# Optimization experiments

Hardware: AMD Instinct MI355X
Metric: run time of the kernel (lower is better)

The kernel has to match this reference:

```python
import jax, jax.numpy as jnp
import numpy as np

NEG_INF = -1e30
EPS = 1e-6


def _apply_rope_interleaved(x, cos, sin):
    # x: (..., rope_dim); cos/sin broadcastable to (..., rope_dim//2)
    x1 = x[..., 0::2]
    x2 = x[..., 1::2]
    o1 = x1 * cos - x2 * sin
    o2 = x1 * sin + x2 * cos
    return jnp.stack([o1, o2], axis=-1).reshape(x.shape)


def setup_inputs() -> dict:
    key = jax.random.key(0)
    ks = jax.random.split(key, 6)
    B, S, D = 1, 2048, 7168
    H, HD, ROPE, QLR = 64, 128, 64, 1536
    x = jax.random.normal(ks[0], (B, S, D), dtype=jnp.float32)
    q_lora = jax.random.normal(ks[1], (B, S, QLR), dtype=jnp.float32)
    wq_b = jax.random.normal(ks[2], (QLR, H * HD), dtype=jnp.float32) * 0.02
    wk = jax.random.normal(ks[3], (D, HD), dtype=jnp.float32) * 0.02
    weights_proj = jax.random.normal(ks[4], (D, H), dtype=jnp.float32) * 0.02
    k_norm_w = jnp.ones((HD,), dtype=jnp.float32)
    k_norm_b = jnp.zeros((HD,), dtype=jnp.float32)
    # standard RoPE tables for the first ROPE dims
    half = ROPE // 2
    inv_freq = 1.0 / (10000.0 ** (np.arange(half, dtype=np.float64) / half))
    ang = np.arange(S, dtype=np.float64)[:, None] * inv_freq[None, :]
    cos = jnp.asarray(np.cos(ang), dtype=jnp.float32)
    sin = jnp.asarray(np.sin(ang), dtype=jnp.float32)
    return {"x": x, "q_lora": q_lora, "wq_b": wq_b, "wk": wk,
            "weights_proj": weights_proj, "k_norm_w": k_norm_w,
            "k_norm_b": k_norm_b, "cos": cos, "sin": sin, "topk": 512}


def reference(x, q_lora, wq_b, wk, weights_proj, k_norm_w, k_norm_b, cos, sin, topk):
    B, S, D = x.shape
    HD = wk.shape[1]
    H = weights_proj.shape[1]
    ROPE = cos.shape[1] * 2
    # queries: low-rank up-projection -> per-head, RoPE on first ROPE dims
    q = (q_lora @ wq_b).reshape(B, S, H, HD)
    q_pe = _apply_rope_interleaved(q[..., :ROPE], cos[None, :, None, :], sin[None, :, None, :])
    q = jnp.concatenate([q_pe, q[..., ROPE:]], axis=-1)
    # keys: single head, LayerNorm then RoPE on first ROPE dims
    k = x @ wk  # [B,S,HD]
    mu = k.mean(-1, keepdims=True)
    var = ((k - mu) ** 2).mean(-1, keepdims=True)
    k = (k - mu) * jax.lax.rsqrt(var + EPS) * k_norm_w + k_norm_b
    k_pe = _apply_rope_interleaved(k[..., :ROPE], cos[None], sin[None])
    k = jnp.concatenate([k_pe, k[..., ROPE:]], axis=-1)
    # per-token head gates, scaled by n_heads^-0.5 and softmax scale HD^-0.5
    w = (x @ weights_proj) * (H ** -0.5) * (HD ** -0.5)  # [B,S,H]
    # lightning index score: I[t,s] = sum_h w[t,h] * relu(q[t,h] . k[s])
    scores = jax.nn.relu(jnp.einsum('bshd,btd->bsht', q, k))  # [B,S,H,S]
    index_score = jnp.einsum('bsht,bsh->bst', scores, w)      # [B,S,S]
    # causal mask then top-k token selection
    causal = jnp.arange(S)[None, :] <= jnp.arange(S)[:, None]
    index_score = jnp.where(causal[None], index_score, NEG_INF)
    vals, idx = jax.lax.top_k(index_score, topk)
    return vals, idx
```

## Files before the change

### kernel.cpp

```cpp
#include <hip/hip_runtime.h>
#include <stdint.h>

#define S_LEN 2048
#define D_DIM 7168
#define H_NUM 64
#define HD_DIM 128
#define QLR_DIM 1536
#define NQ_DIM 8192
#define ROPE_DIM 64
#define HALF_DIM 32
#define TOPK_N 512
#define NEG_INF_F (-1e30f)
#define LN_EPS 1e-6f
#define W_SCALE 0.011048543456039806f

#define KCHUNKS 7
#define KCHUNK_SZ 1024

#define QF_HSTRIDE (128 * 4 * 64 * 8)

#define QBF_OFF 0
#define ALORA_OFF (QBF_OFF + S_LEN * NQ_DIM / 2)
#define WT_OFF   (ALORA_OFF + S_LEN * QLR_DIM / 2)
#define XBF_OFF  (WT_OFF + NQ_DIM * QLR_DIM / 2)
#define WT2_OFF  (XBF_OFF + S_LEN * D_DIM / 2)
#define KF_OFF   (WT2_OFF + 192 * D_DIM / 2)
#define KBF_OFF  (KF_OFF + S_LEN * HD_DIM)
#define WF_OFF   (KBF_OFF + S_LEN * HD_DIM / 2)
#define SC_OFF   (WF_OFF + S_LEN * H_NUM)

typedef __attribute__((ext_vector_type(8))) short short8;
typedef __attribute__((ext_vector_type(4))) float floatx4;

__device__ __forceinline__ ushort f2bf(float f) {
    unsigned int u = __float_as_uint(f);
    u += 0x7FFFu + ((u >> 16) & 1u);
    return (ushort)(u >> 16);
}
__device__ __forceinline__ unsigned int pack2bf(float lo, float hi) {
    return (unsigned int)f2bf(lo) | ((unsigned int)f2bf(hi) << 16);
}

__device__ __forceinline__ void gld_lds16(const ushort* g, ushort* l) {
    __builtin_amdgcn_global_load_lds(
        (const __attribute__((address_space(1))) unsigned int*)g,
        (__attribute__((address_space(3))) unsigned int*)l, 16, 0, 0);
}

__global__ __launch_bounds__(256) void cast_bf16_kernel(
    const float* __restrict__ in, ushort* __restrict__ out)
{
    int g = (blockIdx.x * 256 + threadIdx.x) * 8;
    float4 a = *(const float4*)&in[g];
    float4 b = *(const float4*)&in[g + 4];
    uint4 v;
    v.x = pack2bf(a.x, a.y); v.y = pack2bf(a.z, a.w);
    v.z = pack2bf(b.x, b.y); v.w = pack2bf(b.z, b.w);
    *(uint4*)&out[g] = v;
}

__global__ __launch_bounds__(256) void transpose_wqb_kernel(
    const float* __restrict__ W, ushort* __restrict__ WT)
{
    __shared__ ushort tl[64][72];
    const int n0 = blockIdx.x * 64, k0 = blockIdx.y * 64;
    const int t = threadIdx.x;
    const int r = t >> 4, c4 = (t & 15) * 4;
#pragma unroll
    for (int u = 0; u < 4; u++) {
        int kk = r + u * 16;
        float4 v = *(const float4*)&W[(size_t)(k0 + kk) * NQ_DIM + n0 + c4];
        tl[c4 + 0][kk] = f2bf(v.x);
        tl[c4 + 1][kk] = f2bf(v.y);
        tl[c4 + 2][kk] = f2bf(v.z);
        tl[c4 + 3][kk] = f2bf(v.w);
    }
    __syncthreads();
#pragma unroll
    for (int u = 0; u < 2; u++) {
        int i = t + u * 256;
        int nr = i >> 3, c8 = (i & 7) * 8;
        uint4 v = *(const uint4*)&tl[nr][c8];
        *(uint4*)&WT[(size_t)(n0 + nr) * QLR_DIM + k0 + c8] = v;
    }
}

__global__ __launch_bounds__(256) void transpose_wkp_kernel(
    const float* __restrict__ WK, const float* __restrict__ WP,
    ushort* __restrict__ WT2)
{
    __shared__ ushort tl[64][72];
    const int ntile = blockIdx.x;
    const int k0 = blockIdx.y * 64;
    const float* src; int ld, cbase;
    if (ntile < 2) { src = WK; ld = HD_DIM; cbase = ntile * 64; }
    else           { src = WP; ld = H_NUM; cbase = 0; }
    const int t = threadIdx.x;
    const int r = t >> 4, c4 = (t & 15) * 4;
#pragma unroll
    for (int u = 0; u < 4; u++) {
        int kk = r + u * 16;
        float4 v = *(const float4*)&src[(size_t)(k0 + kk) * ld + cbase + c4];
        tl[c4 + 0][kk] = f2bf(v.x);
        tl[c4 + 1][kk] = f2bf(v.y);
        tl[c4 + 2][kk] = f2bf(v.z);
        tl[c4 + 3][kk] = f2bf(v.w);
    }
    __syncthreads();
#pragma unroll
    for (int u = 0; u < 2; u++) {
        int i = t + u * 256;
        int nr = i >> 3, c8 = (i & 7) * 8;
        uint4 v = *(const uint4*)&tl[nr][c8];
        *(uint4*)&WT2[(size_t)(ntile * 64 + nr) * D_DIM + k0 + c8] = v;
    }
}

__global__ __launch_bounds__(256) void qgemm_mfma_kernel(
    const ushort* __restrict__ Abf,
    const ushort* __restrict__ WT,
    const float* __restrict__ cosp, const float* __restrict__ sinp,
    ushort* __restrict__ Qo)
{
    __shared__ ushort lds[128 * 136];
    ushort* As = lds;
    ushort* Bs = lds + 4096;

    const int tid = threadIdx.x;
    const int lane = tid & 63;
    const int wave = tid >> 6;
    const int m = lane & 15;
    const int q = lane >> 4;
    const int wm = wave & 1, wn = wave >> 1;
    const int m0 = blockIdx.y * 128;
    const int n0 = blockIdx.x * 128;
    const int h = blockIdx.x;

    floatx4 acc[4][4];
#pragma unroll
    for (int i = 0; i < 4; i++)
#pragma unroll
        for (int j = 0; j < 4; j++) acc[i][j] = (floatx4){0.f, 0.f, 0.f, 0.f};

    const ushort* agp[2];
    const ushort* bgp[2];
    unsigned int sbase[2];
#pragma unroll
    for (int u = 0; u < 2; u++) {
        int s = (u * 4 + wave) * 64 + lane;
        agp[u] = Abf + (size_t)(m0 + (s >> 2)) * QLR_DIM + (s & 3) * 8;
        bgp[u] = WT + (size_t)(n0 + (s >> 2)) * QLR_DIM + (s & 3) * 8;
        sbase[u] = (unsigned int)((u * 4 + wave) * 64 * 8);
    }

    for (int kt = 0; kt < QLR_DIM; kt += 32) {
        __syncthreads();
#pragma unroll
        for (int u = 0; u < 2; u++) gld_lds16(agp[u] + kt, &As[sbase[u]]);
#pragma unroll
        for (int u = 0; u < 2; u++) gld_lds16(bgp[u] + kt, &Bs[sbase[u]]);
        __syncthreads();

        short8 af[4], bf[4];
#pragma unroll
        for (int mt = 0; mt < 4; mt++)
            af[mt] = *(const short8*)&As[(wm * 64 + mt * 16 + m) * 32 + q * 8];
#pragma unroll
        for (int nt = 0; nt < 4; nt++)
            bf[nt] = *(const short8*)&Bs[(wn * 64 + nt * 16 + m) * 32 + q * 8];
#pragma unroll
        for (int mt = 0; mt < 4; mt++)
#pragma unroll
            for (int nt = 0; nt < 4; nt++)
                acc[mt][nt] = __builtin_amdgcn_mfma_f32_16x16x32_bf16(
                    af[mt], bf[nt], acc[mt][nt], 0, 0, 0);
    }

    __syncthreads();
    ushort* ep = lds;

#pragma unroll
    for (int mt = 0; mt < 4; mt++) {
        const int srow_base = m0 + wm * 64 + mt * 16 + q * 4;
#pragma unroll
        for (int nt = 0; nt < 4; nt++) {
            const int d = wn * 64 + nt * 16 + m;
            float o[4];
            if (wn == 0) {
                const int jj = d >> 1;
#pragma unroll
                for (int r = 0; r < 4; r++) {
                    float x = acc[mt][nt][r];
                    float p = __shfl_xor(x, 1, 64);
                    float c = cosp[(srow_base + r) * HALF_DIM + jj];
                    float sn = sinp[(srow_base + r) * HALF_DIM + jj];
                    o[r] = (d & 1) ? (p * sn + x * c) : (x * c - p * sn);
                }
            } else {
#pragma unroll
                for (int r = 0; r < 4; r++) o[r] = acc[mt][nt][r];
            }
#pragma unroll
            for (int r = 0; r < 4; r++)
                ep[(wm * 64 + mt * 16 + q * 4 + r) * 136 + d] = f2bf(o[r]);
        }
    }
    __syncthreads();

    const int sgrp0 = m0 >> 4;
#pragma unroll
    for (int u = 0; u < 8; u++) {
        int i = u * 256 + tid;
        int sgl = i >> 8, c = i & 255;
        int ks = c >> 6, ln = c & 63;
        int srow = sgl * 16 + (ln & 15);
        int d0 = (ks << 5) + ((ln >> 4) << 3);
        uint4 v = *(const uint4*)&ep[srow * 136 + d0];
        size_t dst = (size_t)h * QF_HSTRIDE +
                     ((((size_t)(sgrp0 + sgl) * 4 + ks) * 64 + ln) * 8);
        *(uint4*)&Qo[dst] = v;
    }
}

__global__ __launch_bounds__(256) void kw_mfma_kernel(
    const ushort* __restrict__ Xbf,
    const ushort* __restrict__ WT2,
    float* __restrict__ partial)
{
    __shared__ ushort As[128 * 64];
    __shared__ ushort Bs[64 * 64];

    const int tid = threadIdx.x;
    const int lane = tid & 63;
    const int wave = tid >> 6;
    const int m = lane & 15;
    const int q = lane >> 4;
    const int wm = wave & 1, wn = wave >> 1;
    const int m0 = blockIdx.x * 128;
    const int n0 = blockIdx.y * 64;
    const int kc = blockIdx.z;
    const size_t kbase = (size_t)kc * KCHUNK_SZ;

    const ushort* agp[4];
    unsigned int abase[4];
#pragma unroll
    for (int u = 0; u < 4; u++) {
        int s = (u * 4 + wave) * 64 + lane;
        int row = s >> 3, c = s & 7;
        int kg = c ^ (row & 7);
        agp[u] = Xbf + (size_t)(m0 + row) * D_DIM + kbase + kg * 8;
        abase[u] = (unsigned int)((u * 4 + wave) * 64 * 8);
    }
    const ushort* bgp[2];
    unsigned int bbase[2];
#pragma unroll
    for (int u = 0; u < 2; u++) {
        int s = (u * 4 + wave) * 64 + lane;
        int row = s >> 3, c = s & 7;
        int kg = c ^ (row & 7);
        bgp[u] = WT2 + (size_t)(n0 + row) * D_DIM + kbase + kg * 8;
        bbase[u] = (unsigned int)((u * 4 + wave) * 64 * 8);
    }

    floatx4 acc[4][2];
#pragma unroll
    for (int i = 0; i < 4; i++)
#pragma unroll
        for (int j = 0; j < 2; j++) acc[i][j] = (floatx4){0.f, 0.f, 0.f, 0.f};

    for (int kt = 0; kt < KCHUNK_SZ; kt += 64) {
        __syncthreads();
#pragma unroll
        for (int u = 0; u < 4; u++) gld_lds16(agp[u] + kt, &As[abase[u]]);
#pragma unroll
        for (int u = 0; u < 2; u++) gld_lds16(bgp[u] + kt, &Bs[bbase[u]]);
        __syncthreads();

        short8 af[4][2], bfr[2][2];
#pragma unroll
        for (int mt = 0; mt < 4; mt++) {
            int row = wm * 64 + mt * 16 + m;
#pragma unroll
            for (int ks = 0; ks < 2; ks++)
                af[mt][ks] = *(const short8*)
                    &As[row * 64 + ((((ks << 2) + q) ^ (m & 7)) * 8)];
        }
#pragma unroll
        for (int nt = 0; nt < 2; nt++) {
            int row = wn * 32 + nt * 16 + m;
#pragma unroll
            for (int ks = 0; ks < 2; ks++)
                bfr[nt][ks] = *(const short8*)
                    &Bs[row * 64 + ((((ks << 2) + q) ^ (m & 7)) * 8)];
        }
#pragma unroll
        for (int mt = 0; mt < 4; mt++)
#pragma unroll
            for (int nt = 0; nt < 2; nt++)
#pragma unroll
                for (int ks = 0; ks < 2; ks++)
                    acc[mt][nt] = __builtin_amdgcn_mfma_f32_16x16x32_bf16(
                        af[mt][ks], bfr[nt][ks], acc[mt][nt], 0, 0, 0);
    }

#pragma unroll
    for (int mt = 0; mt < 4; mt++) {
        int grow = m0 + wm * 64 + mt * 16 + q * 4;
#pragma unroll
        for (int nt = 0; nt < 2; nt++) {
            int gn = n0 + wn * 32 + nt * 16 + m;
#pragma unroll
            for (int r = 0; r < 4; r++)
                partial[((size_t)kc * S_LEN + grow + r) * 192 + gn] = acc[mt][nt][r];
        }
    }
}

__global__ __launch_bounds__(256) void kw_reduce_kernel(
    const float* __restrict__ partial, float* __restrict__ Ko, float* __restrict__ Wo)
{
    int g = blockIdx.x * 256 + threadIdx.x;
    int m = g / 192, n = g % 192;
    float s = 0.f;
#pragma unroll
    for (int c = 0; c < KCHUNKS; c++)
        s += partial[((size_t)c * S_LEN + m) * 192 + n];
    if (n < HD_DIM) Ko[(size_t)m * HD_DIM + n] = s;
    else            Wo[(size_t)m * H_NUM + (n - HD_DIM)] = s * W_SCALE;
}

__global__ __launch_bounds__(128) void knorm_rope_kernel(
    const float* __restrict__ Kf, const float* __restrict__ gw, const float* __restrict__ gb,
    const float* __restrict__ cosp, const float* __restrict__ sinp,
    ushort* __restrict__ Kbf)
{
    __shared__ float red[128];
    __shared__ float sh[128];
    const int m = blockIdx.x, t = threadIdx.x;
    float v = Kf[(size_t)m * HD_DIM + t];
    red[t] = v; __syncthreads();
    for (int off = 64; off > 0; off >>= 1) {
        if (t < off) red[t] += red[t + off];
        __syncthreads();
    }
    float mu = red[0] * (1.f / HD_DIM);
    __syncthreads();
    float dv = v - mu;
    red[t] = dv * dv; __syncthreads();
    for (int off = 64; off > 0; off >>= 1) {
        if (t < off) red[t] += red[t + off];
        __syncthreads();
    }
    float var = red[0] * (1.f / HD_DIM);
    float rs = rsqrtf(var + LN_EPS);
    float kn = dv * rs * gw[t] + gb[t];
    sh[t] = kn; __syncthreads();
    float out;
    if (t < ROPE_DIM) {
        int jj = t >> 1;
        float c = cosp[m * HALF_DIM + jj], sn = sinp[m * HALF_DIM + jj];
        out = ((t & 1) == 0) ? (sh[t] * c - sh[t + 1] * sn)
                             : (sh[t - 1] * sn + sh[t] * c);
    } else {
        out = kn;
    }
    Kbf[(size_t)m * HD_DIM + t] = f2bf(out);
}

__global__ __launch_bounds__(256, 2) void attn_mfma_kernel(
    const ushort* __restrict__ Qb,
    const ushort* __restrict__ Kb,
    const float* __restrict__ Wf,
    float* __restrict__ SC)
{
    __shared__ float Wsm[64 * 68];

    const int bidx = blockIdx.x;
    const int x = bidx & 7, j = bidx >> 3;
    const int g1 = x + 1, g2 = 32 - x, g3 = x + 9;
    int ts, tt;
    if (j < g1)                { ts = x;      tt = j; }
    else if (j < g1 + g2)      { ts = 31 - x; tt = j - g1; }
    else if (j < g1 + g2 + g3) { ts = x + 8;  tt = j - g1 - g2; }
    else                       { ts = 23 - x; tt = j - g1 - g2 - g3; }
    const int s0 = ts * 64, t0 = tt * 64;

    const int tid = threadIdx.x;
    const int lane = tid & 63;
    const int m = lane & 15;
    const int q = lane >> 4;
    const int strip = (tid >> 6) * 16;

    {
        const float4* gw = (const float4*)(Wf + (size_t)s0 * H_NUM);
#pragma unroll
        for (int u = 0; u < 4; u++) {
            int ch = tid + u * 256;
            float4 v = gw[ch];
            *(float4*)&Wsm[(ch >> 4) * 68 + (ch & 15) * 4] = v;
        }
    }

    short8 bf[4][4];
#pragma unroll
    for (int tile = 0; tile < 4; tile++)
#pragma unroll
        for (int ks = 0; ks < 4; ks++)
            bf[tile][ks] = *(const short8*)
                &Kb[(size_t)(t0 + tile * 16 + m) * HD_DIM + ks * 32 + q * 8];

    __syncthreads();

    float acc[4][4];
#pragma unroll
    for (int tile = 0; tile < 4; tile++)
#pragma unroll
        for (int r = 0; r < 4; r++) acc[tile][r] = 0.f;

    const int sgrp = ts * 4 + (strip >> 4);
    const ushort* qfb = Qb + ((size_t)sgrp * 4 * 64 + lane) * 8;
    const float* wrow = &Wsm[(strip + q * 4) * 68];

    auto loadQ = [&](short8* dst, int h) {
        const ushort* p = qfb + (size_t)h * QF_HSTRIDE;
#pragma unroll
        for (int ks = 0; ks < 4; ks++) dst[ks] = *(const short8*)&p[ks * 512];
    };
    auto computeH = [&](const short8* af, int h) {
        float wv[4];
#pragma unroll
        for (int r = 0; r < 4; r++) wv[r] = wrow[r * 68 + h];
#pragma unroll
        for (int tile = 0; tile < 4; tile++) {
            floatx4 p = {0.f, 0.f, 0.f, 0.f};
#pragma unroll
            for (int ks = 0; ks < 4; ks++)
                p = __builtin_amdgcn_mfma_f32_16x16x32_bf16(af[ks], bf[tile][ks], p, 0, 0, 0);
#pragma unroll
            for (int r = 0; r < 4; r++)
                acc[tile][r] += fmaxf(p[r], 0.f) * wv[r];
        }
    };

    short8 afA[4], afB[4];
    loadQ(afA, 0);
    for (int h = 0; h < H_NUM; h += 2) {
        loadQ(afB, h + 1);
        computeH(afA, h);
        if (h + 2 < H_NUM) loadQ(afA, h + 2);
        computeH(afB, h + 1);
    }

#pragma unroll
    for (int tile = 0; tile < 4; tile++)
#pragma unroll
        for (int r = 0; r < 4; r++)
            SC[(size_t)(s0 + strip + q * 4 + r) * S_LEN + t0 + tile * 16 + m] =
                acc[tile][r];
}

__device__ __forceinline__ unsigned int fkey(float f) {
    unsigned int u = __float_as_uint(f);
    return (u & 0x80000000u) ? ~u : (u | 0x80000000u);
}
__device__ __forceinline__ float fdec(unsigned int k) {
    unsigned int u = (k & 0x80000000u) ? (k & 0x7FFFFFFFu) : ~k;
    return __uint_as_float(u);
}

__global__ __launch_bounds__(256) void topk_kernel(
    const float* __restrict__ SC, float* __restrict__ outv, float* __restrict__ outi)
{
    __shared__ unsigned long long key[S_LEN];
    const int s = blockIdx.x, tid = threadIdx.x;
    for (int t = tid; t < S_LEN; t += 256) {
        float v = (t <= s) ? SC[(size_t)s * S_LEN + t] : NEG_INF_F;
        key[t] = ((unsigned long long)fkey(v) << 32) |
                 (unsigned long long)(unsigned int)(S_LEN - 1 - t);
    }
    __syncthreads();
    for (int k2 = 2; k2 <= S_LEN; k2 <<= 1) {
        for (int j = k2 >> 1; j > 0; j >>= 1) {
            for (int p = tid; p < S_LEN / 2; p += 256) {
                int i = 2 * p - (p & (j - 1));
                int ix = i + j;
                unsigned long long a = key[i], b = key[ix];
                bool up = ((i & k2) == 0);
                bool sw = up ? (a < b) : (a > b);
                if (sw) { key[i] = b; key[ix] = a; }
            }
            __syncthreads();
        }
    }
    for (int i2 = tid; i2 < TOPK_N; i2 += 256) {
        unsigned long long kv = key[i2];
        outv[(size_t)s * TOPK_N + i2] = fdec((unsigned int)(kv >> 32));
        outi[(size_t)s * TOPK_N + i2] =
            (float)(S_LEN - 1 - (int)(kv & 0xFFFFFFFFu));
    }
}

extern "C" void kernel_launch(void* const* d_in, const int* in_sizes, int n_in,
                              void* d_out, int out_size, void* d_ws, size_t ws_size,
                              hipStream_t stream)
{
    (void)in_sizes; (void)n_in; (void)out_size; (void)ws_size;
    const float* x      = (const float*)d_in[0];
    const float* q_lora = (const float*)d_in[1];
    const float* wq_b   = (const float*)d_in[2];
    const float* wk     = (const float*)d_in[3];
    const float* wproj  = (const float*)d_in[4];
    const float* knw    = (const float*)d_in[5];
    const float* knb    = (const float*)d_in[6];
    const float* cosp   = (const float*)d_in[7];
    const float* sinp   = (const float*)d_in[8];

    float* ws = (float*)d_ws;
    ushort* Qbf  = (ushort*)(ws + QBF_OFF);
    ushort* Albf = (ushort*)(ws + ALORA_OFF);
    ushort* WTbf = (ushort*)(ws + WT_OFF);
    ushort* Xbf  = (ushort*)(ws + XBF_OFF);
    ushort* WT2  = (ushort*)(ws + WT2_OFF);
    float*  Kf   = ws + KF_OFF;
    ushort* Kbf  = (ushort*)(ws + KBF_OFF);
    float*  Wf   = ws + WF_OFF;
    float*  SCb  = ws + SC_OFF;
    float*  partial = ws + SC_OFF;

    float* outv = (float*)d_out;
    float* outi = outv + (size_t)S_LEN * TOPK_N;

    cast_bf16_kernel<<<(S_LEN * QLR_DIM) / (256 * 8), 256, 0, stream>>>(q_lora, Albf);
    cast_bf16_kernel<<<(S_LEN * D_DIM) / (256 * 8), 256, 0, stream>>>(x, Xbf);
    transpose_wqb_kernel<<<dim3(NQ_DIM / 64, QLR_DIM / 64), 256, 0, stream>>>(wq_b, WTbf);
    transpose_wkp_kernel<<<dim3(3, D_DIM / 64), 256, 0, stream>>>(wk, wproj, WT2);
    kw_mfma_kernel<<<dim3(S_LEN / 128, 3, KCHUNKS), 256, 0, stream>>>(Xbf, WT2, partial);
    kw_reduce_kernel<<<(S_LEN * 192) / 256, 256, 0, stream>>>(partial, Kf, Wf);
    knorm_rope_kernel<<<S_LEN, 128, 0, stream>>>(Kf, knw, knb, cosp, sinp, Kbf);
    qgemm_mfma_kernel<<<dim3(NQ_DIM / 128, S_LEN / 128), 256, 0, stream>>>(
        Albf, WTbf, cosp, sinp, Qbf);
    attn_mfma_kernel<<<528, 256, 0, stream>>>(Qbf, Kbf, Wf, SCb);
    topk_kernel<<<S_LEN, 256, 0, stream>>>(SCb, outv, outi);
}
```

Measured before the change: 401.8 us.

## Replace full bitonic sort with chunked 512-sort and merge using 32-bit packed keys

The top-k kernel now sorts only the causally active prefix of each row, split into 512-element chunks. Each chunk is bitonic-sorted, then chunks are merged pairwise keeping the top 512. Keys shrink from 64-bit to 32-bit by packing a truncated float key with an 11-bit index, and output values are read back from a saved value array. This cuts shared-memory traffic and sort stages, especially for early rows. In exchange, ordering can deviate when scores differ only in the truncated low mantissa bits.

Result: faster. 361.1 us (-10.1%).

```diff
diff --git a/kernel.cpp b/kernel.cpp
--- a/kernel.cpp
+++ b/kernel.cpp
@@ -463,40 +463,57 @@
     unsigned int u = __float_as_uint(f);
     return (u & 0x80000000u) ? ~u : (u | 0x80000000u);
 }
-__device__ __forceinline__ float fdec(unsigned int k) {
-    unsigned int u = (k & 0x80000000u) ? (k & 0x7FFFFFFFu) : ~k;
-    return __uint_as_float(u);
-}
 
 __global__ __launch_bounds__(256) void topk_kernel(
     const float* __restrict__ SC, float* __restrict__ outv, float* __restrict__ outi)
 {
-    __shared__ unsigned long long key[S_LEN];
+    __shared__ unsigned int key[S_LEN];
+    __shared__ float val[S_LEN];
     const int s = blockIdx.x, tid = threadIdx.x;
-    for (int t = tid; t < S_LEN; t += 256) {
+    const int nchunks = (s >> 9) + 1;
+    const int nact = nchunks << 9;
+
+    for (int t = tid; t < nact; t += 256) {
         float v = (t <= s) ? SC[(size_t)s * S_LEN + t] : NEG_INF_F;
-        key[t] = ((unsigned long long)fkey(v) << 32) |
-                 (unsigned long long)(unsigned int)(S_LEN - 1 - t);
-    }
-    __syncthreads();
-    for (int k2 = 2; k2 <= S_LEN; k2 <<= 1) {
+        val[t] = v;
+        key[t] = (fkey(v) & 0xFFFFF800u) | (unsigned int)(S_LEN - 1 - t);
+    }
+    __syncthreads();
+
+    for (int k2 = 2; k2 <= 512; k2 <<= 1) {
         for (int j = k2 >> 1; j > 0; j >>= 1) {
-            for (int p = tid; p < S_LEN / 2; p += 256) {
+            for (int p = tid; p < (nact >> 1); p += 256) {
                 int i = 2 * p - (p & (j - 1));
-                int ix = i + j;
-                unsigned long long a = key[i], b = key[ix];
-                bool up = ((i & k2) == 0);
+                int il = i & 511;
+                unsigned int a = key[i], b = key[i + j];
+                bool up = ((il & k2) == 0);
                 bool sw = up ? (a < b) : (a > b);
-                if (sw) { key[i] = b; key[ix] = a; }
+                if (sw) { key[i] = b; key[i + j] = a; }
             }
             __syncthreads();
         }
     }
+
+    for (int c = 1; c < nchunks; c++) {
+        for (int p = tid; p < 512; p += 256) {
+            unsigned int a = key[p], b = key[(c << 9) + 511 - p];
+            key[p] = a > b ? a : b;
+        }
+        __syncthreads();
+        for (int j = 256; j > 0; j >>= 1) {
+            int p = tid;
+            int i = 2 * p - (p & (j - 1));
+            unsigned int a = key[i], b = key[i + j];
+            if (a < b) { key[i] = b; key[i + j] = a; }
+            __syncthreads();
+        }
+    }
+
     for (int i2 = tid; i2 < TOPK_N; i2 += 256) {
-        unsigned long long kv = key[i2];
-        outv[(size_t)s * TOPK_N + i2] = fdec((unsigned int)(kv >> 32));
-        outi[(size_t)s * TOPK_N + i2] =
-            (float)(S_LEN - 1 - (int)(kv & 0xFFFFFFFFu));
+        unsigned int kv = key[i2];
+        int t = S_LEN - 1 - (int)(kv & 0x7FFu);
+        outv[(size_t)s * TOPK_N + i2] = val[t];
+        outi[(size_t)s * TOPK_N + i2] = (float)t;
     }
 }
 
```
